# Optimization experiments

Measured on AMD Instinct MI355X. Metric: run time of the kernel, lower is better.

Reference implementation:

```python
import jax, jax.numpy as jnp
import numpy as np

B, C, H, W_SP = 64, 16, 8, 8
IN_DIM, MIDDLE, NUM_CLASSES = 2048, 8192, 2048
K_ITERS, TAU, NUM_GROUPS = 1024, 0.5, 8
SPLIT = NUM_GROUPS * 7 * 7  # 392
BN_EPS = 1e-5


def setup_inputs() -> dict:
    key = jax.random.key(0)
    ks = jax.random.split(key, 20)
    f = jax.random.normal(ks[0], (B, C, H, W_SP), jnp.float32)

    def lin(kw, kb, fan_out, fan_in):
        lim = 1.0 / np.sqrt(fan_in)
        W = jax.random.uniform(kw, (fan_out, fan_in), jnp.float32, -lim, lim)
        b = jax.random.uniform(kb, (fan_out,), jnp.float32, -lim, lim)
        return W, b

    def bn_stats(km, kv, n):
        rm = 0.1 * jax.random.normal(km, (n,), jnp.float32)
        rv = jax.random.uniform(kv, (n,), jnp.float32, 0.5, 1.5)
        return rm, rv

    W1, b1 = lin(ks[1], ks[2], MIDDLE, IN_DIM)
    g1 = 1.0 + 0.1 * jax.random.normal(ks[3], (MIDDLE,), jnp.float32)
    beta1 = 0.1 * jax.random.normal(ks[4], (MIDDLE,), jnp.float32)
    rm1, rv1 = bn_stats(ks[5], ks[6], MIDDLE)

    W2, b2 = lin(ks[7], ks[8], MIDDLE, MIDDLE)
    g2 = 1.0 + 0.1 * jax.random.normal(ks[9], (MIDDLE,), jnp.float32)
    beta2 = 0.1 * jax.random.normal(ks[10], (MIDDLE,), jnp.float32)
    rm2, rv2 = bn_stats(ks[11], ks[12], MIDDLE)

    W3, b3 = lin(ks[13], ks[14], NUM_CLASSES, MIDDLE)
    rm3, rv3 = bn_stats(ks[15], ks[16], NUM_CLASSES)  # final BN, affine=False

    return {"f": f, "W1": W1, "b1": b1, "g1": g1, "beta1": beta1, "rm1": rm1, "rv1": rv1,
            "W2": W2, "b2": b2, "g2": g2, "beta2": beta2, "rm2": rm2, "rv2": rv2,
            "W3": W3, "b3": b3, "rm3": rm3, "rv3": rv3}


def _bn(x, rm, rv, g=None, b=None):
    y = (x - rm) / jnp.sqrt(rv + BN_EPS)
    if g is not None:
        y = y * g + b
    return y


def reference(f, W1, b1, g1, beta1, rm1, rv1, W2, b2, g2, beta2, rm2, rv2, W3, b3, rm3, rv3):
    # FFT over spatial axes; the original code overwrites abs/angle with the raw
    # complex array twice, then the torch dtype cast drops the imaginary part.
    f_fft = jnp.fft.fft2(f, axes=(2, 3))
    flat = jnp.real(f_fft).reshape(B, -1).astype(f.dtype)  # [64, 1024]
    x = jnp.concatenate([flat, flat], axis=1)              # [64, 2048]

    # MLP in eval mode (Dropout = identity, BatchNorm uses running stats)
    h = jax.nn.relu(_bn(x @ W1.T + b1, rm1, rv1, g1, beta1))
    h = jax.nn.relu(_bn(h @ W2.T + b2, rm2, rv2, g2, beta2))
    mask = _bn(h @ W3.T + b3, rm3, rv3)                    # [64, 2048]

    # Iterated gumbel-softmax with running max, k=1024 iterations
    keys = jax.random.split(jax.random.key(42), K_ITERS)
    tiny = jnp.finfo(mask.dtype).tiny

    def step(carry, k):
        m, z = carry
        u = jax.random.uniform(k, m.shape, m.dtype, minval=tiny, maxval=1.0)
        gum = -jnp.log(-jnp.log(u))
        m = jax.nn.softmax((m + gum) / TAU, axis=1)
        z = jnp.maximum(m, z)
        return (m, z), None

    (_, z), _ = jax.lax.scan(step, (mask, jnp.zeros_like(mask)), keys)
    return z[:, :SPLIT], z[:, SPLIT:]
```

## Files before the change

### kernel.cpp

```cpp
#include <hip/hip_runtime.h>
#include <hip/hip_bf16.h>
#include <stdint.h>

__device__ __forceinline__ uint32_t rotl32(uint32_t v, int s) {
    return (v << s) | (v >> (32 - s));
}

__device__ __forceinline__ void tf2x32(uint32_t k0, uint32_t k1,
                                       uint32_t x0, uint32_t x1,
                                       uint32_t& o0, uint32_t& o1) {
    uint32_t ks2 = k0 ^ k1 ^ 0x1BD11BDAu;
    x0 += k0; x1 += k1;
#define TFR(R0,R1,R2,R3) \
    x0 += x1; x1 = rotl32(x1, R0); x1 ^= x0; \
    x0 += x1; x1 = rotl32(x1, R1); x1 ^= x0; \
    x0 += x1; x1 = rotl32(x1, R2); x1 ^= x0; \
    x0 += x1; x1 = rotl32(x1, R3); x1 ^= x0;
    TFR(13,15,26,6)   x0 += k1;  x1 += ks2 + 1u;
    TFR(17,29,16,24)  x0 += ks2; x1 += k0  + 2u;
    TFR(13,15,26,6)   x0 += k0;  x1 += k1  + 3u;
    TFR(17,29,16,24)  x0 += k1;  x1 += ks2 + 4u;
    TFR(13,15,26,6)   x0 += ks2; x1 += k0  + 5u;
#undef TFR
    o0 = x0; o1 = x1;
}

__device__ __forceinline__ uint32_t pbits32(uint32_t k0, uint32_t k1, uint32_t ctr) {
    uint32_t o0, o1;
    tf2x32(k0, k1, 0u, ctr, o0, o1);
    return o0 ^ o1;
}

#define NROW 64
#define NCOL 2048
#define NFLAT 131072
#define SPLIT 392
#define C2 2.8853900817779268f

__device__ __forceinline__ float gumbel_from_bits(uint32_t bits) {
    const float TINY = 1.17549435e-38f;
    float f = (float)(bits >> 9) * 1.1920928955078125e-7f;
    float u = fmaxf(TINY, f + TINY);
    return -logf(-logf(u));
}

__global__ __launch_bounds__(256) void keygenF(uint32_t* __restrict__ kb) {
    int n = blockIdx.x * 256 + threadIdx.x;
    uint32_t o0, o1;
    tf2x32(0u, 42u, 0u, (uint32_t)n, o0, o1);
    kb[2 * n] = o0;
    kb[2 * n + 1] = o1;
}

__device__ __constant__ float c_ctab[8] = {
    1.0f, 0.70710678118654752f, 0.0f, -0.70710678118654752f,
   -1.0f, -0.70710678118654752f, 0.0f, 0.70710678118654752f
};

__global__ __launch_bounds__(256) void fft_x(const float* __restrict__ f,
                                             float* __restrict__ x) {
    int gid = blockIdx.x * 256 + threadIdx.x;
    int b = gid >> 10, i = gid & 1023;
    int c = i >> 6, h = (i >> 3) & 7, w = i & 7;
    const float* fb = f + ((b << 4) + c) * 64;
    float s = 0.0f;
#pragma unroll
    for (int hp = 0; hp < 8; ++hp) {
#pragma unroll
        for (int wp = 0; wp < 8; ++wp)
            s += fb[hp * 8 + wp] * c_ctab[(h * hp + w * wp) & 7];
    }
    x[b * NCOL + i] = s;
    x[b * NCOL + 1024 + i] = s;
}

__global__ __launch_bounds__(256) void prep(
    const float* __restrict__ b1, const float* __restrict__ g1,
    const float* __restrict__ be1, const float* __restrict__ rm1, const float* __restrict__ rv1,
    const float* __restrict__ b2, const float* __restrict__ g2,
    const float* __restrict__ be2, const float* __restrict__ rm2, const float* __restrict__ rv2,
    float* __restrict__ s1, float* __restrict__ o1,
    float* __restrict__ s2, float* __restrict__ o2) {
    int i = blockIdx.x * 256 + threadIdx.x;
    const float eps = 1e-5f;
    float inv = 1.0f / sqrtf(rv1[i] + eps);
    float s = g1[i] * inv;
    s1[i] = s; o1[i] = (b1[i] - rm1[i]) * s + be1[i];
    inv = 1.0f / sqrtf(rv2[i] + eps);
    s = g2[i] * inv;
    s2[i] = s; o2[i] = (b2[i] - rm2[i]) * s + be2[i];
}

template<bool AFF>
__global__ __launch_bounds__(256)
void gemm_ks(const float* __restrict__ A,
             const float* __restrict__ sA, const float* __restrict__ oA,
             const float* __restrict__ B, float* __restrict__ Cpart,
             int K, int Kc, int N) {
    __shared__ float As[32][68];
    __shared__ float Bs[32][132];
    const int t = threadIdx.x;
    const int n0 = blockIdx.x * 128;
    const int k0 = blockIdx.y * Kc;
    const int tm = t >> 4, tn = t & 15;

    float acc[4][8];
#pragma unroll
    for (int i = 0; i < 4; ++i)
#pragma unroll
        for (int j = 0; j < 8; ++j) acc[i][j] = 0.0f;

    for (int kt = k0; kt < k0 + Kc; kt += 32) {
#pragma unroll
        for (int h = 0; h < 2; ++h) {
            int idx = h * 1024 + t * 4;
            int am = idx >> 5, ak = idx & 31;
            size_t go = (size_t)am * K + kt + ak;
            float4 v = *(const float4*)(A + go);
            if (AFF) {
                float4 s = *(const float4*)(sA + kt + ak);
                float4 o = *(const float4*)(oA + kt + ak);
                v.x = fmaxf(v.x * s.x + o.x, 0.0f);
                v.y = fmaxf(v.y * s.y + o.y, 0.0f);
                v.z = fmaxf(v.z * s.z + o.z, 0.0f);
                v.w = fmaxf(v.w * s.w + o.w, 0.0f);
            }
            As[ak + 0][am] = v.x; As[ak + 1][am] = v.y;
            As[ak + 2][am] = v.z; As[ak + 3][am] = v.w;
        }
#pragma unroll
        for (int h = 0; h < 4; ++h) {
            int idx = h * 1024 + t * 4;
            int bn = idx >> 5, bk = idx & 31;
            float4 v = *(const float4*)(B + (size_t)(n0 + bn) * K + kt + bk);
            Bs[bk + 0][bn] = v.x; Bs[bk + 1][bn] = v.y;
            Bs[bk + 2][bn] = v.z; Bs[bk + 3][bn] = v.w;
        }
        __syncthreads();
#pragma unroll 8
        for (int kk = 0; kk < 32; ++kk) {
            float4 av = *(const float4*)&As[kk][tm << 2];
            float4 b0 = *(const float4*)&Bs[kk][tn << 3];
            float4 b1 = *(const float4*)&Bs[kk][(tn << 3) + 4];
            float a4[4] = {av.x, av.y, av.z, av.w};
            float b8[8] = {b0.x, b0.y, b0.z, b0.w, b1.x, b1.y, b1.z, b1.w};
#pragma unroll
            for (int i = 0; i < 4; ++i)
#pragma unroll
                for (int j = 0; j < 8; ++j)
                    acc[i][j] = fmaf(a4[i], b8[j], acc[i][j]);
        }
        __syncthreads();
    }
#pragma unroll
    for (int i = 0; i < 4; ++i) {
        size_t co = (size_t)blockIdx.y * ((size_t)64 * N)
                  + (size_t)((tm << 2) + i) * N + n0 + (tn << 3);
        float4 v0 = {acc[i][0], acc[i][1], acc[i][2], acc[i][3]};
        float4 v1 = {acc[i][4], acc[i][5], acc[i][6], acc[i][7]};
        *(float4*)(Cpart + co) = v0;
        *(float4*)(Cpart + co + 4) = v1;
    }
}

__global__ __launch_bounds__(256) void combineP(const float* __restrict__ parts,
                                                float* __restrict__ dst,
                                                int P, int total) {
    int gid = blockIdx.x * 256 + threadIdx.x;
    if (gid >= total) return;
    float s = 0.0f;
    for (int p = 0; p < P; ++p) s += parts[(size_t)p * total + gid];
    dst[gid] = s;
}

__global__ __launch_bounds__(256) void combine3(const float* __restrict__ parts,
                                                const float* __restrict__ b3,
                                                const float* __restrict__ rm3,
                                                const float* __restrict__ rv3,
                                                float* __restrict__ mstate, int P) {
    int gid = blockIdx.x * 256 + threadIdx.x;
    int c = gid & 2047;
    float v = 0.0f;
    for (int p = 0; p < P; ++p) v += parts[(size_t)p * NFLAT + gid];
    mstate[gid] = (v + b3[c] - rm3[c]) / sqrtf(rv3[c] + 1e-5f);
}

__global__ __launch_bounds__(1024)
void hash_chunk(const uint32_t* __restrict__ kb, float* __restrict__ gbuf,
                int t0, int Tc) {
    size_t total = (size_t)Tc * NFLAT;
    for (size_t idx = (size_t)blockIdx.x * 1024 + threadIdx.x; idx < total;
         idx += (size_t)gridDim.x * 1024) {
        int tt = (int)(idx >> 17);
        int j  = (int)(idx & (NFLAT - 1));
        int tg = t0 + tt;
        uint32_t k0 = kb[2 * tg], k1 = kb[2 * tg + 1];
        gbuf[idx] = gumbel_from_bits(pbits32(k0, k1, (uint32_t)j)) * C2;
    }
}

__global__ __launch_bounds__(1024)
void scan_fused(float* __restrict__ mstate, float* __restrict__ zstate,
                const float* __restrict__ gbufA, float* __restrict__ gbufB,
                const uint32_t* __restrict__ kb,
                int t0, int Tc, int last, float* __restrict__ out) {
    __shared__ __align__(16) float red[2][16];
    const int tid = threadIdx.x;

    if (blockIdx.x < 64) {
        const int r = blockIdx.x;
        const int c0 = tid, c1 = tid + 1024;
        const int base = r * NCOL;
        float m0 = mstate[base + c0], m1 = mstate[base + c1];
        float z0, z1;
        if (t0 == 0) { z0 = 0.0f; z1 = 0.0f; }
        else         { z0 = zstate[base + c0]; z1 = zstate[base + c1]; }
        const int lane = tid & 63, wid = tid >> 6;

        float g0 = gbufA[base + c0];
        float g1 = gbufA[base + c1];
        for (int tt = 0; tt < Tc; ++tt) {
            float cg0 = g0, cg1 = g1;
            if (tt + 1 < Tc) {
                size_t ao = (size_t)(tt + 1) * NFLAT + base;
                g0 = gbufA[ao + c0];
                g1 = gbufA[ao + c1];
            }
            float p0 = exp2f(fmaf(m0, C2, cg0));
            float p1 = exp2f(fmaf(m1, C2, cg1));
            float ps = p0 + p1;
#pragma unroll
            for (int d = 1; d < 64; d <<= 1) ps += __shfl_xor(ps, d, 64);
            if (lane == 0) red[tt & 1][wid] = ps;
            __syncthreads();
            float S;
            {
                const float4* r4 = (const float4*)&red[tt & 1][0];
                float4 v0 = r4[0], v1 = r4[1], v2 = r4[2], v3 = r4[3];
                S = ((v0.x + v0.y) + (v0.z + v0.w)) + ((v1.x + v1.y) + (v1.z + v1.w))
                  + ((v2.x + v2.y) + (v2.z + v2.w)) + ((v3.x + v3.y) + (v3.z + v3.w));
            }
            float rs = __builtin_amdgcn_rcpf(S);
            m0 = p0 * rs; m1 = p1 * rs;
            z0 = fmaxf(z0, m0); z1 = fmaxf(z1, m1);
        }
        mstate[base + c0] = m0; mstate[base + c1] = m1;
        zstate[base + c0] = z0; zstate[base + c1] = z1;
        if (last) {
            if (c0 < SPLIT) out[r * SPLIT + c0] = z0;
            else out[64 * SPLIT + r * (NCOL - SPLIT) + (c0 - SPLIT)] = z0;
            out[64 * SPLIT + r * (NCOL - SPLIT) + (c1 - SPLIT)] = z1;
        }
    } else if (!last) {
        int hb = blockIdx.x - 64;
        int tbase = t0 + Tc;
        size_t total = (size_t)Tc * NFLAT;
        for (size_t idx = (size_t)hb * 1024 + tid; idx < total;
             idx += (size_t)192 * 1024) {
            int tt = (int)(idx >> 17);
            int j  = (int)(idx & (NFLAT - 1));
            int tg = tbase + tt;
            uint32_t k0 = kb[2 * tg], k1 = kb[2 * tg + 1];
            gbufB[idx] = gumbel_from_bits(pbits32(k0, k1, (uint32_t)j)) * C2;
        }
    }
}

__global__ __launch_bounds__(1024)
void scan_inline(const float* __restrict__ mstate, const uint32_t* __restrict__ kb,
                 float* __restrict__ out) {
    const int r = blockIdx.x;
    const int tid = threadIdx.x;
    const int c0 = tid, c1 = tid + 1024;
    const int base = r * NCOL;
    float m0 = mstate[base + c0], m1 = mstate[base + c1];
    float z0 = 0.0f, z1 = 0.0f;
    __shared__ __align__(16) float red[2][16];
    const int lane = tid & 63, wid = tid >> 6;

    for (int t = 0; t < 1024; ++t) {
        uint32_t k0 = kb[2 * t], k1 = kb[2 * t + 1];
        float g0 = gumbel_from_bits(pbits32(k0, k1, (uint32_t)(base + c0)));
        float g1 = gumbel_from_bits(pbits32(k0, k1, (uint32_t)(base + c1)));
        float p0 = exp2f((m0 + g0) * C2);
        float p1 = exp2f((m1 + g1) * C2);
        float ps = p0 + p1;
#pragma unroll
        for (int d = 1; d < 64; d <<= 1) ps += __shfl_xor(ps, d, 64);
        if (lane == 0) red[t & 1][wid] = ps;
        __syncthreads();
        float S;
        {
            const float4* r4 = (const float4*)&red[t & 1][0];
            float4 v0 = r4[0], v1 = r4[1], v2 = r4[2], v3 = r4[3];
            S = ((v0.x + v0.y) + (v0.z + v0.w)) + ((v1.x + v1.y) + (v1.z + v1.w))
              + ((v2.x + v2.y) + (v2.z + v2.w)) + ((v3.x + v3.y) + (v3.z + v3.w));
        }
        float rs = __builtin_amdgcn_rcpf(S);
        m0 = p0 * rs; m1 = p1 * rs;
        z0 = fmaxf(z0, m0); z1 = fmaxf(z1, m1);
    }
    if (c0 < SPLIT) out[r * SPLIT + c0] = z0;
    else out[64 * SPLIT + r * (NCOL - SPLIT) + (c0 - SPLIT)] = z0;
    out[64 * SPLIT + r * (NCOL - SPLIT) + (c1 - SPLIT)] = z1;
}

extern "C" void kernel_launch(void* const* d_in, const int* in_sizes, int n_in,
                              void* d_out, int out_size, void* d_ws, size_t ws_size,
                              hipStream_t stream) {
    const float* f   = (const float*)d_in[0];
    const float* W1  = (const float*)d_in[1];
    const float* b1  = (const float*)d_in[2];
    const float* g1  = (const float*)d_in[3];
    const float* be1 = (const float*)d_in[4];
    const float* rm1 = (const float*)d_in[5];
    const float* rv1 = (const float*)d_in[6];
    const float* W2  = (const float*)d_in[7];
    const float* b2  = (const float*)d_in[8];
    const float* g2  = (const float*)d_in[9];
    const float* be2 = (const float*)d_in[10];
    const float* rm2 = (const float*)d_in[11];
    const float* rv2 = (const float*)d_in[12];
    const float* W3  = (const float*)d_in[13];
    const float* b3  = (const float*)d_in[14];
    const float* rm3 = (const float*)d_in[15];
    const float* rv3 = (const float*)d_in[16];
    float* out = (float*)d_out;

    float* ws = (float*)d_ws;
    size_t off = 0;
    auto alloc = [&](size_t n) { float* p = ws + off; off += n; return p; };

    uint32_t* keybuf = (uint32_t*)alloc(2048);
    float* s1 = alloc(8192); float* o1 = alloc(8192);
    float* s2 = alloc(8192); float* o2 = alloc(8192);
    float* x      = alloc(64 * 2048);
    float* h1     = alloc((size_t)64 * 8192);
    float* h2     = alloc((size_t)64 * 8192);
    float* mstate = alloc(NFLAT);
    float* zstate = alloc(NFLAT);
    size_t fixed = off;
    float* pbuf = ws + fixed;
    size_t region = (ws_size / 4 > fixed) ? (ws_size / 4 - fixed) : 0;

    const size_t HN = (size_t)64 * 8192;
    int KS1 = (region >= 8 * HN) ? 8 : (region >= 4 * HN) ? 4 :
              (region >= 2 * HN) ? 2 : 1;
    int KS2 = (region >= 16 * HN) ? 16 : (region >= 8 * HN) ? 8 :
              (region >= 4 * HN) ? 4 : (region >= 2 * HN) ? 2 : 1;
    int KS3 = (region >= 16 * (size_t)NFLAT) ? 16 : (region >= 8 * (size_t)NFLAT) ? 8 :
              (region >= 4 * (size_t)NFLAT) ? 4 : (region >= 2 * (size_t)NFLAT) ? 2 : 1;

    int Tc = 0;
    const int cands[5] = {128, 64, 32, 16, 8};
    for (int ci = 0; ci < 5; ++ci)
        if (2 * (size_t)cands[ci] * NFLAT <= region) { Tc = cands[ci]; break; }

    keygenF<<<dim3(4), 256, 0, stream>>>(keybuf);
    prep<<<dim3(32), 256, 0, stream>>>(b1, g1, be1, rm1, rv1,
                                       b2, g2, be2, rm2, rv2,
                                       s1, o1, s2, o2);
    fft_x<<<dim3(256), 256, 0, stream>>>(f, x);

    if (KS1 > 1) {
        gemm_ks<false><<<dim3(64, KS1), 256, 0, stream>>>(
            x, nullptr, nullptr, W1, pbuf, 2048, 2048 / KS1, 8192);
        combineP<<<dim3(2048), 256, 0, stream>>>(pbuf, h1, KS1, (int)HN);
    } else {
        gemm_ks<false><<<dim3(64, 1), 256, 0, stream>>>(
            x, nullptr, nullptr, W1, h1, 2048, 2048, 8192);
    }
    if (KS2 > 1) {
        gemm_ks<true><<<dim3(64, KS2), 256, 0, stream>>>(
            h1, s1, o1, W2, pbuf, 8192, 8192 / KS2, 8192);
        combineP<<<dim3(2048), 256, 0, stream>>>(pbuf, h2, KS2, (int)HN);
    } else {
        gemm_ks<true><<<dim3(64, 1), 256, 0, stream>>>(
            h1, s1, o1, W2, h2, 8192, 8192, 8192);
    }
    if (KS3 > 1) {
        gemm_ks<true><<<dim3(16, KS3), 256, 0, stream>>>(
            h2, s2, o2, W3, pbuf, 8192, 8192 / KS3, 2048);
        combine3<<<dim3(512), 256, 0, stream>>>(pbuf, b3, rm3, rv3, mstate, KS3);
    } else {
        gemm_ks<true><<<dim3(16, 1), 256, 0, stream>>>(
            h2, s2, o2, W3, h1, 8192, 8192, 2048);
        combine3<<<dim3(512), 256, 0, stream>>>(h1, b3, rm3, rv3, mstate, 1);
    }

    if (Tc > 0) {
        float* gbuf0 = pbuf;
        float* gbuf1 = pbuf + (size_t)Tc * NFLAT;
        int NC = 1024 / Tc;
        hash_chunk<<<dim3(256), 1024, 0, stream>>>(keybuf, gbuf0, 0, Tc);
        for (int ch = 0; ch < NC; ++ch) {
            float* ga = (ch & 1) ? gbuf1 : gbuf0;
            float* gb = (ch & 1) ? gbuf0 : gbuf1;
            scan_fused<<<dim3(256), 1024, 0, stream>>>(
                mstate, zstate, ga, gb, keybuf,
                ch * Tc, Tc, (ch == NC - 1) ? 1 : 0, out);
        }
    } else {
        scan_inline<<<dim3(64), 1024, 0, stream>>>(mstate, keybuf, out);
    }
}
```

Before: 992.0 us.

## Overlap gumbel hashing with GEMMs, swizzle GEMM smem, DPP wave reduction

When the workspace is large enough, the Gumbel noise for the first 512 scan steps is generated by extra blocks launched alongside the three MLP GEMMs, which now use a flattened 1D grid. The scan kernels generate the remaining steps into one large buffer instead of double-buffering. The GEMM shared-memory tiles are stored k-contiguous with an XOR swizzle and read as float4 along k. The softmax wave reduction uses DPP instead of shuffles. This needs a 512MB noise buffer, and the hash blocks may compete with the GEMM blocks for compute units.

```diff
diff --git a/kernel.cpp b/kernel.cpp
--- a/kernel.cpp
+++ b/kernel.cpp
@@ -44,6 +44,24 @@
     return -logf(-logf(u));
 }
 
+template<int CTRL, int RM>
+__device__ __forceinline__ float dpp_add(float s) {
+    int x = __builtin_amdgcn_update_dpp(0, __builtin_bit_cast(int, s),
+                                        CTRL, RM, 0xf, true);
+    return s + __builtin_bit_cast(float, x);
+}
+
+__device__ __forceinline__ float wave_sum64(float v) {
+    v = dpp_add<0x111, 0xf>(v);
+    v = dpp_add<0x112, 0xf>(v);
+    v = dpp_add<0x114, 0xf>(v);
+    v = dpp_add<0x118, 0xf>(v);
+    v = dpp_add<0x142, 0xa>(v);
+    v = dpp_add<0x143, 0xc>(v);
+    return __builtin_bit_cast(float,
+        __builtin_amdgcn_readlane(__builtin_bit_cast(int, v), 63));
+}
+
 __global__ __launch_bounds__(256) void keygenF(uint32_t* __restrict__ kb) {
     int n = blockIdx.x * 256 + threadIdx.x;
     uint32_t o0, o1;
@@ -93,15 +111,34 @@
 
 template<bool AFF>
 __global__ __launch_bounds__(256)
-void gemm_ks(const float* __restrict__ A,
-             const float* __restrict__ sA, const float* __restrict__ oA,
-             const float* __restrict__ B, float* __restrict__ Cpart,
-             int K, int Kc, int N) {
-    __shared__ float As[32][68];
-    __shared__ float Bs[32][132];
+void gemm_hash(const float* __restrict__ A,
+               const float* __restrict__ sA, const float* __restrict__ oA,
+               const float* __restrict__ B, float* __restrict__ Cpart,
+               int K, int Kc, int N, int gemmBlocks,
+               const uint32_t* __restrict__ kb2, float* __restrict__ hdst,
+               int ht0, int hcnt) {
+    if ((int)blockIdx.x >= gemmBlocks) {
+        if (hcnt <= 0) return;
+        int hb = blockIdx.x - gemmBlocks;
+        int hBlocks = gridDim.x - gemmBlocks;
+        size_t total = (size_t)hcnt * NFLAT;
+        for (size_t idx = (size_t)hb * 256 + threadIdx.x; idx < total;
+             idx += (size_t)hBlocks * 256) {
+            int tt = (int)(idx >> 17);
+            int j  = (int)(idx & (NFLAT - 1));
+            int tg = ht0 + tt;
+            uint32_t k0 = kb2[2 * tg], k1 = kb2[2 * tg + 1];
+            hdst[idx] = gumbel_from_bits(pbits32(k0, k1, (uint32_t)j)) * C2;
+        }
+        return;
+    }
+
+    __shared__ __align__(16) float As[64 * 36];
+    __shared__ __align__(16) float Bs[128 * 36];
     const int t = threadIdx.x;
-    const int n0 = blockIdx.x * 128;
-    const int k0 = blockIdx.y * Kc;
+    const int nb = N >> 7;
+    const int n0 = (blockIdx.x % nb) * 128;
+    const int k0 = (blockIdx.x / nb) * Kc;
     const int tm = t >> 4, tn = t & 15;
 
     float acc[4][8];
@@ -115,8 +152,7 @@
         for (int h = 0; h < 2; ++h) {
             int idx = h * 1024 + t * 4;
             int am = idx >> 5, ak = idx & 31;
-            size_t go = (size_t)am * K + kt + ak;
-            float4 v = *(const float4*)(A + go);
+            float4 v = *(const float4*)(A + (size_t)am * K + kt + ak);
             if (AFF) {
                 float4 s = *(const float4*)(sA + kt + ak);
                 float4 o = *(const float4*)(oA + kt + ak);
@@ -125,36 +161,42 @@
                 v.z = fmaxf(v.z * s.z + o.z, 0.0f);
                 v.w = fmaxf(v.w * s.w + o.w, 0.0f);
             }
-            As[ak + 0][am] = v.x; As[ak + 1][am] = v.y;
-            As[ak + 2][am] = v.z; As[ak + 3][am] = v.w;
+            *(float4*)&As[am * 36 + (ak ^ (((am >> 2) & 7) << 2))] = v;
         }
 #pragma unroll
         for (int h = 0; h < 4; ++h) {
             int idx = h * 1024 + t * 4;
             int bn = idx >> 5, bk = idx & 31;
             float4 v = *(const float4*)(B + (size_t)(n0 + bn) * K + kt + bk);
-            Bs[bk + 0][bn] = v.x; Bs[bk + 1][bn] = v.y;
-            Bs[bk + 2][bn] = v.z; Bs[bk + 3][bn] = v.w;
+            *(float4*)&Bs[bn * 36 + (bk ^ (((bn >> 3) & 7) << 2))] = v;
         }
         __syncthreads();
-#pragma unroll 8
-        for (int kk = 0; kk < 32; ++kk) {
-            float4 av = *(const float4*)&As[kk][tm << 2];
-            float4 b0 = *(const float4*)&Bs[kk][tn << 3];
-            float4 b1 = *(const float4*)&Bs[kk][(tn << 3) + 4];
-            float a4[4] = {av.x, av.y, av.z, av.w};
-            float b8[8] = {b0.x, b0.y, b0.z, b0.w, b1.x, b1.y, b1.z, b1.w};
+#pragma unroll
+        for (int kbk = 0; kbk < 8; ++kbk) {
+            float4 a[4], b[8];
+            int acol = (kbk * 4) ^ ((tm & 7) << 2);
 #pragma unroll
             for (int i = 0; i < 4; ++i)
-#pragma unroll
-                for (int j = 0; j < 8; ++j)
-                    acc[i][j] = fmaf(a4[i], b8[j], acc[i][j]);
+                a[i] = *(const float4*)&As[(tm * 4 + i) * 36 + acol];
+            int bcol = (kbk * 4) ^ ((tn & 7) << 2);
+#pragma unroll
+            for (int j = 0; j < 8; ++j)
+                b[j] = *(const float4*)&Bs[(tn * 8 + j) * 36 + bcol];
+#pragma unroll
+            for (int i = 0; i < 4; ++i)
+#pragma unroll
+                for (int j = 0; j < 8; ++j) {
+                    acc[i][j] = fmaf(a[i].x, b[j].x, acc[i][j]);
+                    acc[i][j] = fmaf(a[i].y, b[j].y, acc[i][j]);
+                    acc[i][j] = fmaf(a[i].z, b[j].z, acc[i][j]);
+                    acc[i][j] = fmaf(a[i].w, b[j].w, acc[i][j]);
+                }
         }
         __syncthreads();
     }
 #pragma unroll
     for (int i = 0; i < 4; ++i) {
-        size_t co = (size_t)blockIdx.y * ((size_t)64 * N)
+        size_t co = (size_t)(blockIdx.x / nb) * ((size_t)64 * N)
                   + (size_t)((tm << 2) + i) * N + n0 + (tn << 3);
         float4 v0 = {acc[i][0], acc[i][1], acc[i][2], acc[i][3]};
         float4 v1 = {acc[i][4], acc[i][5], acc[i][6], acc[i][7]};
@@ -201,68 +243,68 @@
 
 __global__ __launch_bounds__(1024)
 void scan_fused(float* __restrict__ mstate, float* __restrict__ zstate,
-                const float* __restrict__ gbufA, float* __restrict__ gbufB,
+                const float* __restrict__ gscan,
+                float* __restrict__ hdst, int ht0, int hcnt,
                 const uint32_t* __restrict__ kb,
                 int t0, int Tc, int last, float* __restrict__ out) {
-    __shared__ __align__(16) float red[2][16];
     const int tid = threadIdx.x;
 
-    if (blockIdx.x < 64) {
-        const int r = blockIdx.x;
-        const int c0 = tid, c1 = tid + 1024;
-        const int base = r * NCOL;
-        float m0 = mstate[base + c0], m1 = mstate[base + c1];
-        float z0, z1;
-        if (t0 == 0) { z0 = 0.0f; z1 = 0.0f; }
-        else         { z0 = zstate[base + c0]; z1 = zstate[base + c1]; }
-        const int lane = tid & 63, wid = tid >> 6;
-
-        float g0 = gbufA[base + c0];
-        float g1 = gbufA[base + c1];
-        for (int tt = 0; tt < Tc; ++tt) {
-            float cg0 = g0, cg1 = g1;
-            if (tt + 1 < Tc) {
-                size_t ao = (size_t)(tt + 1) * NFLAT + base;
-                g0 = gbufA[ao + c0];
-                g1 = gbufA[ao + c1];
-            }
-            float p0 = exp2f(fmaf(m0, C2, cg0));
-            float p1 = exp2f(fmaf(m1, C2, cg1));
-            float ps = p0 + p1;
-#pragma unroll
-            for (int d = 1; d < 64; d <<= 1) ps += __shfl_xor(ps, d, 64);
-            if (lane == 0) red[tt & 1][wid] = ps;
-            __syncthreads();
-            float S;
-            {
-                const float4* r4 = (const float4*)&red[tt & 1][0];
-                float4 v0 = r4[0], v1 = r4[1], v2 = r4[2], v3 = r4[3];
-                S = ((v0.x + v0.y) + (v0.z + v0.w)) + ((v1.x + v1.y) + (v1.z + v1.w))
-                  + ((v2.x + v2.y) + (v2.z + v2.w)) + ((v3.x + v3.y) + (v3.z + v3.w));
-            }
-            float rs = __builtin_amdgcn_rcpf(S);
-            m0 = p0 * rs; m1 = p1 * rs;
-            z0 = fmaxf(z0, m0); z1 = fmaxf(z1, m1);
-        }
-        mstate[base + c0] = m0; mstate[base + c1] = m1;
-        zstate[base + c0] = z0; zstate[base + c1] = z1;
-        if (last) {
-            if (c0 < SPLIT) out[r * SPLIT + c0] = z0;
-            else out[64 * SPLIT + r * (NCOL - SPLIT) + (c0 - SPLIT)] = z0;
-            out[64 * SPLIT + r * (NCOL - SPLIT) + (c1 - SPLIT)] = z1;
-        }
-    } else if (!last) {
+    if (blockIdx.x >= 64) {
+        if (hcnt <= 0) return;
         int hb = blockIdx.x - 64;
-        int tbase = t0 + Tc;
-        size_t total = (size_t)Tc * NFLAT;
+        size_t total = (size_t)hcnt * NFLAT;
         for (size_t idx = (size_t)hb * 1024 + tid; idx < total;
              idx += (size_t)192 * 1024) {
             int tt = (int)(idx >> 17);
             int j  = (int)(idx & (NFLAT - 1));
-            int tg = tbase + tt;
+            int tg = ht0 + tt;
             uint32_t k0 = kb[2 * tg], k1 = kb[2 * tg + 1];
-            gbufB[idx] = gumbel_from_bits(pbits32(k0, k1, (uint32_t)j)) * C2;
-        }
+            hdst[idx] = gumbel_from_bits(pbits32(k0, k1, (uint32_t)j)) * C2;
+        }
+        return;
+    }
+
+    __shared__ __align__(16) float red[2][16];
+    const int r = blockIdx.x;
+    const int c0 = tid, c1 = tid + 1024;
+    const int base = r * NCOL;
+    float m0 = mstate[base + c0], m1 = mstate[base + c1];
+    float z0, z1;
+    if (t0 == 0) { z0 = 0.0f; z1 = 0.0f; }
+    else         { z0 = zstate[base + c0]; z1 = zstate[base + c1]; }
+    const int lane = tid & 63, wid = tid >> 6;
+
+    float g0 = gscan[base + c0];
+    float g1 = gscan[base + c1];
+    for (int tt = 0; tt < Tc; ++tt) {
+        float cg0 = g0, cg1 = g1;
+        if (tt + 1 < Tc) {
+            size_t ao = (size_t)(tt + 1) * NFLAT + base;
+            g0 = gscan[ao + c0];
+            g1 = gscan[ao + c1];
+        }
+        float p0 = exp2f(fmaf(m0, C2, cg0));
+        float p1 = exp2f(fmaf(m1, C2, cg1));
+        float ws = wave_sum64(p0 + p1);
+        if (lane == 0) red[tt & 1][wid] = ws;
+        __syncthreads();
+        float S;
+        {
+            const float4* r4 = (const float4*)&red[tt & 1][0];
+            float4 v0 = r4[0], v1 = r4[1], v2 = r4[2], v3 = r4[3];
+            S = ((v0.x + v0.y) + (v0.z + v0.w)) + ((v1.x + v1.y) + (v1.z + v1.w))
+              + ((v2.x + v2.y) + (v2.z + v2.w)) + ((v3.x + v3.y) + (v3.z + v3.w));
+        }
+        float rs = __builtin_amdgcn_rcpf(S);
+        m0 = p0 * rs; m1 = p1 * rs;
+        z0 = fmaxf(z0, m0); z1 = fmaxf(z1, m1);
+    }
+    mstate[base + c0] = m0; mstate[base + c1] = m1;
+    zstate[base + c0] = z0; zstate[base + c1] = z1;
+    if (last) {
+        if (c0 < SPLIT) out[r * SPLIT + c0] = z0;
+        else out[64 * SPLIT + r * (NCOL - SPLIT) + (c0 - SPLIT)] = z0;
+        out[64 * SPLIT + r * (NCOL - SPLIT) + (c1 - SPLIT)] = z1;
     }
 }
 
@@ -344,17 +386,7 @@
     size_t region = (ws_size / 4 > fixed) ? (ws_size / 4 - fixed) : 0;
 
     const size_t HN = (size_t)64 * 8192;
-    int KS1 = (region >= 8 * HN) ? 8 : (region >= 4 * HN) ? 4 :
-              (region >= 2 * HN) ? 2 : 1;
-    int KS2 = (region >= 16 * HN) ? 16 : (region >= 8 * HN) ? 8 :
-              (region >= 4 * HN) ? 4 : (region >= 2 * HN) ? 2 : 1;
-    int KS3 = (region >= 16 * (size_t)NFLAT) ? 16 : (region >= 8 * (size_t)NFLAT) ? 8 :
-              (region >= 4 * (size_t)NFLAT) ? 4 : (region >= 2 * (size_t)NFLAT) ? 2 : 1;
-
-    int Tc = 0;
-    const int cands[5] = {128, 64, 32, 16, 8};
-    for (int ci = 0; ci < 5; ++ci)
-        if (2 * (size_t)cands[ci] * NFLAT <= region) { Tc = cands[ci]; break; }
+    const size_t GALL = (size_t)1024 * NFLAT;
 
     keygenF<<<dim3(4), 256, 0, stream>>>(keybuf);
     prep<<<dim3(32), 256, 0, stream>>>(b1, g1, be1, rm1, rv1,
@@ -362,45 +394,81 @@
                                        s1, o1, s2, o2);
     fft_x<<<dim3(256), 256, 0, stream>>>(f, x);
 
-    if (KS1 > 1) {
-        gemm_ks<false><<<dim3(64, KS1), 256, 0, stream>>>(
-            x, nullptr, nullptr, W1, pbuf, 2048, 2048 / KS1, 8192);
-        combineP<<<dim3(2048), 256, 0, stream>>>(pbuf, h1, KS1, (int)HN);
+    if (region >= GALL + 16 * HN) {
+        float* gbufAll = pbuf;
+        float* parts   = pbuf + GALL;
+
+        gemm_hash<false><<<dim3(512 + 256), 256, 0, stream>>>(
+            x, nullptr, nullptr, W1, parts, 2048, 256, 8192, 512,
+            keybuf, gbufAll, 0, 128);
+        combineP<<<dim3(2048), 256, 0, stream>>>(parts, h1, 8, (int)HN);
+        gemm_hash<true><<<dim3(1024 + 256), 256, 0, stream>>>(
+            h1, s1, o1, W2, parts, 8192, 512, 8192, 1024,
+            keybuf, gbufAll + (size_t)128 * NFLAT, 128, 256);
+        combineP<<<dim3(2048), 256, 0, stream>>>(parts, h2, 16, (int)HN);
+        gemm_hash<true><<<dim3(256 + 256), 256, 0, stream>>>(
+            h2, s2, o2, W3, parts, 8192, 512, 2048, 256,
+            keybuf, gbufAll + (size_t)384 * NFLAT, 384, 128);
+        combine3<<<dim3(512), 256, 0, stream>>>(parts, b3, rm3, rv3, mstate, 16);
+
+        for (int ch = 0; ch < 8; ++ch) {
+            int hstart = 512 + ch * 128;
+            int hcnt = (hstart < 1024) ? 128 : 0;
+            scan_fused<<<dim3(256), 1024, 0, stream>>>(
+                mstate, zstate, gbufAll + (size_t)ch * 128 * NFLAT,
+                gbufAll + (size_t)hstart * NFLAT, hstart, hcnt, keybuf,
+                ch * 128, 128, (ch == 7) ? 1 : 0, out);
+        }
     } else {
-        gemm_ks<false><<<dim3(64, 1), 256, 0, stream>>>(
-            x, nullptr, nullptr, W1, h1, 2048, 2048, 8192);
-    }
-    if (KS2 > 1) {
-        gemm_ks<true><<<dim3(64, KS2), 256, 0, stream>>>(
-            h1, s1, o1, W2, pbuf, 8192, 8192 / KS2, 8192);
-        combineP<<<dim3(2048), 256, 0, stream>>>(pbuf, h2, KS2, (int)HN);
-    } else {
-        gemm_ks<true><<<dim3(64, 1), 256, 0, stream>>>(
-            h1, s1, o1, W2, h2, 8192, 8192, 8192);
-    }
-    if (KS3 > 1) {
-        gemm_ks<true><<<dim3(16, KS3), 256, 0, stream>>>(
-            h2, s2, o2, W3, pbuf, 8192, 8192 / KS3, 2048);
-        combine3<<<dim3(512), 256, 0, stream>>>(pbuf, b3, rm3, rv3, mstate, KS3);
-    } else {
-        gemm_ks<true><<<dim3(16, 1), 256, 0, stream>>>(
-            h2, s2, o2, W3, h1, 8192, 8192, 2048);
-        combine3<<<dim3(512), 256, 0, stream>>>(h1, b3, rm3, rv3, mstate, 1);
-    }
-
-    if (Tc > 0) {
-        float* gbuf0 = pbuf;
-        float* gbuf1 = pbuf + (size_t)Tc * NFLAT;
-        int NC = 1024 / Tc;
-        hash_chunk<<<dim3(256), 1024, 0, stream>>>(keybuf, gbuf0, 0, Tc);
-        for (int ch = 0; ch < NC; ++ch) {
-            float* ga = (ch & 1) ? gbuf1 : gbuf0;
-            float* gb = (ch & 1) ? gbuf0 : gbuf1;
-            scan_fused<<<dim3(256), 1024, 0, stream>>>(
-                mstate, zstate, ga, gb, keybuf,
-                ch * Tc, Tc, (ch == NC - 1) ? 1 : 0, out);
-        }
-    } else {
-        scan_inline<<<dim3(64), 1024, 0, stream>>>(mstate, keybuf, out);
-    }
-}
+        int KS1 = (region >= 8 * HN) ? 8 : (region >= 4 * HN) ? 4 :
+                  (region >= 2 * HN) ? 2 : 1;
+        int KS2 = (region >= 16 * HN) ? 16 : (region >= 8 * HN) ? 8 :
+                  (region >= 4 * HN) ? 4 : (region >= 2 * HN) ? 2 : 1;
+        int KS3 = (region >= 16 * (size_t)NFLAT) ? 16 :
+                  (region >= 8 * (size_t)NFLAT) ? 8 :
+                  (region >= 4 * (size_t)NFLAT) ? 4 :
+                  (region >= 2 * (size_t)NFLAT) ? 2 : 1;
+        int Tc = 0;
+        const int cands[5] = {128, 64, 32, 16, 8};
+        for (int ci = 0; ci < 5; ++ci)
+            if (2 * (size_t)cands[ci] * NFLAT <= region) { Tc = cands[ci]; break; }
+
+        gemm_hash<false><<<dim3(64 * KS1), 256, 0, stream>>>(
+            x, nullptr, nullptr, W1, (KS1 > 1) ? pbuf : h1,
+            2048, 2048 / KS1, 8192, 64 * KS1, keybuf, nullptr, 0, 0);
+        if (KS1 > 1) combineP<<<dim3(2048), 256, 0, stream>>>(pbuf, h1, KS1, (int)HN);
+
+        gemm_hash<true><<<dim3(64 * KS2), 256, 0, stream>>>(
+            h1, s1, o1, W2, (KS2 > 1) ? pbuf : h2,
+            8192, 8192 / KS2, 8192, 64 * KS2, keybuf, nullptr, 0, 0);
+        if (KS2 > 1) combineP<<<dim3(2048), 256, 0, stream>>>(pbuf, h2, KS2, (int)HN);
+
+        if (KS3 > 1) {
+            gemm_hash<true><<<dim3(16 * KS3), 256, 0, stream>>>(
+                h2, s2, o2, W3, pbuf, 8192, 8192 / KS3, 2048, 16 * KS3,
+                keybuf, nullptr, 0, 0);
+            combine3<<<dim3(512), 256, 0, stream>>>(pbuf, b3, rm3, rv3, mstate, KS3);
+        } else {
+            gemm_hash<true><<<dim3(16), 256, 0, stream>>>(
+                h2, s2, o2, W3, h1, 8192, 8192, 2048, 16, keybuf, nullptr, 0, 0);
+            combine3<<<dim3(512), 256, 0, stream>>>(h1, b3, rm3, rv3, mstate, 1);
+        }
+
+        if (Tc > 0) {
+            float* gbuf0 = pbuf;
+            float* gbuf1 = pbuf + (size_t)Tc * NFLAT;
+            int NC = 1024 / Tc;
+            hash_chunk<<<dim3(256), 1024, 0, stream>>>(keybuf, gbuf0, 0, Tc);
+            for (int ch = 0; ch < NC; ++ch) {
+                float* ga = (ch & 1) ? gbuf1 : gbuf0;
+                float* gb = (ch & 1) ? gbuf0 : gbuf1;
+                int last = (ch == NC - 1) ? 1 : 0;
+                scan_fused<<<dim3(256), 1024, 0, stream>>>(
+                    mstate, zstate, ga, gb, (ch + 1) * Tc, last ? 0 : Tc,
+                    keybuf, ch * Tc, Tc, last, out);
+            }
+        } else {
+            scan_inline<<<dim3(64), 1024, 0, stream>>>(mstate, keybuf, out);
+        }
+    }
+}
```

After: 1.188 ms. 19.7% more time.
